# Kernel tuning notes

Measured on AMD Instinct MI355X. Metric: run time of the kernel, lower is better.

Reference implementation:

```python
import jax, jax.numpy as jnp
import numpy as np
import math

INF = 10000000000.0
D_KEY = 64


def setup_inputs() -> dict:
    key = jax.random.key(0)
    kq, kk, kv = jax.random.split(key, 3)
    B, S, D = 4, 4096, D_KEY
    return {
        "query": jax.random.normal(kq, (B, S, D), dtype=jnp.float32),
        "key": jax.random.normal(kk, (B, S, D), dtype=jnp.float32),
        "value": jax.random.normal(kv, (B, S, D), dtype=jnp.float32),
    }


def reference(query, key, value):
    # dot_products: [B, Sq, Sk]
    scale = math.sqrt(D_KEY)
    scores = jnp.einsum("bqd,bkd->bqk", query, key)
    S = key.shape[1]
    # causal: subtract INF on strict upper triangle (triu(1)), before scaling
    tri = jnp.triu(jnp.full((S, S), INF, dtype=scores.dtype), k=1)
    scores = scores - tri[None, :, :]
    logits = scores / scale
    probs = jax.nn.softmax(logits, axis=-1)  # softmax over key dim
    # dropout p=0.0 -> identity
    return jnp.einsum("bqk,bkd->bqd", probs, value)
```

## Files before the change

### kernel.cpp

```cpp
#include <hip/hip_runtime.h>
#include <hip/hip_bf16.h>
#include <math.h>

#define B_  4
#define S_  4096
#define D_  64
#define NQT 64
#define NST 32
#define QSC 0.18033688f
#define M0  20.0f

typedef __attribute__((ext_vector_type(8))) short bf16x8;
typedef __attribute__((ext_vector_type(4))) float f32x4;
typedef __attribute__((ext_vector_type(4))) short short4v;

static __device__ inline short f2bf(float f) {
    union { float f; unsigned u; } v; v.f = f;
    unsigned u = v.u;
    unsigned r = u + 0x7fff + ((u >> 16) & 1);
    return (short)(r >> 16);
}
static __device__ inline float bf2f(short s) {
    union { unsigned u; float f; } v; v.u = ((unsigned)(unsigned short)s) << 16;
    return v.f;
}
static __device__ inline unsigned cvt_pk_bf16(float lo, float hi) {
    unsigned r;
    asm("v_cvt_pk_bf16_f32 %0, %1, %2" : "=v"(r) : "v"(lo), "v"(hi));
    return r;
}
static __device__ inline void gload_lds16(const void* g, void* l) {
    __builtin_amdgcn_global_load_lds(
        (const __attribute__((address_space(1))) unsigned int*)g,
        (__attribute__((address_space(3))) unsigned int*)l,
        16, 0, 0);
}

__global__ __launch_bounds__(256) void fa_prep(const float* __restrict__ K,
                                               const float* __restrict__ V,
                                               short* __restrict__ Kbf,
                                               short* __restrict__ Vtbf)
{
    const int b   = blockIdx.x >> 6;
    const int st  = blockIdx.x & 63;
    const int tid = threadIdx.x;
    __shared__ short Vs[64 * 72];

    const size_t tbase = ((size_t)b * S_ + (size_t)st * 64) * D_;
    #pragma unroll
    for (int rr = 0; rr < 4; ++rr) {
        int i = tid + rr * 256;
        size_t e = tbase + (size_t)i * 4;
        f32x4 k = *(const f32x4*)(K + e);
        union { short4v s; unsigned u[2]; } ks;
        ks.u[0] = cvt_pk_bf16(k[0], k[1]);
        ks.u[1] = cvt_pk_bf16(k[2], k[3]);
        int key = i >> 4, d4 = (i & 15) * 4;
        int d4s = (((d4 >> 3) ^ (key & 7)) << 3) + (d4 & 7);
        *(short4v*)(Kbf + tbase + (size_t)key * 64 + d4s) = ks.s;
        f32x4 v = *(const f32x4*)(V + e);
        int slot = (key & 32) + (((key & 15) >> 2) << 3) + (((key >> 4) & 1) << 2) + (key & 3);
        Vs[(d4 + 0) * 72 + slot] = f2bf(v[0]);
        Vs[(d4 + 1) * 72 + slot] = f2bf(v[1]);
        Vs[(d4 + 2) * 72 + slot] = f2bf(v[2]);
        Vs[(d4 + 3) * 72 + slot] = f2bf(v[3]);
    }
    __syncthreads();
    #pragma unroll
    for (int cc = 0; cc < 2; ++cc) {
        int c = tid + cc * 256;
        int d = c >> 3, sg = c & 7;
        bf16x8 row = *(const bf16x8*)&Vs[d * 72 + sg * 8];
        *(bf16x8*)(Vtbf + ((size_t)(b * D_ + d)) * S_ + (size_t)st * 64 + (sg ^ (d & 7)) * 8) = row;
    }
}

__global__ __launch_bounds__(512, 6) void fa_part(const float* __restrict__ Qf,
                                               const short* __restrict__ Kbf,
                                               const short* __restrict__ Vtbf,
                                               short* __restrict__ Opart,
                                               float* __restrict__ Lpart,
                                               int CH, int T)
{
    const int bid = blockIdx.x;
    const int b   = bid / T;
    int r = bid - b * T;
    int qt2 = NST - 1;
    while (true) {
        int n = (2 * qt2 + 2 + CH - 1) / CH;
        if (r < n) break;
        r -= n; --qt2;
    }
    const int kt0 = r * CH;
    const int nkt = 2 * qt2 + 2;
    const int kt1 = (kt0 + CH < nkt) ? kt0 + CH : nkt;

    const int tid  = threadIdx.x;
    const int wave = tid >> 6;
    const int lane = tid & 63;
    const int lm   = lane & 15;
    const int lk   = lane >> 4;

    __shared__ __align__(16) short Ks[2][64 * 64];
    __shared__ __align__(16) short Vt[2][64 * 64];

    bf16x8 qA[2];
    {
        const float* qp = Qf + ((size_t)(b * S_ + qt2 * 128 + wave * 16 + lm)) * D_;
        #pragma unroll
        for (int h = 0; h < 2; ++h) {
            f32x4 a0 = *(const f32x4*)(qp + h * 32 + lk * 8);
            f32x4 a1 = *(const f32x4*)(qp + h * 32 + lk * 8 + 4);
            union { bf16x8 v; unsigned u[4]; } qa;
            qa.u[0] = cvt_pk_bf16(a0[0] * QSC, a0[1] * QSC);
            qa.u[1] = cvt_pk_bf16(a0[2] * QSC, a0[3] * QSC);
            qa.u[2] = cvt_pk_bf16(a1[0] * QSC, a1[1] * QSC);
            qa.u[3] = cvt_pk_bf16(a1[2] * QSC, a1[3] * QSC);
            qA[h] = qa.v;
        }
    }

    bf16x8 onesF;
    #pragma unroll
    for (int j = 0; j < 8; ++j) onesF[j] = (short)0x3F80;

    const char* kgp = (const char*)(Kbf + (size_t)b * S_ * D_)
                    + (size_t)kt0 * 8192 + tid * 16;
    const char* vgp = (const char*)(Vtbf + ((size_t)(b * D_ + (tid >> 3))) * S_)
                    + (size_t)kt0 * 128 + (tid & 7) * 16;

    gload_lds16(kgp, &Ks[0][wave * 512]);
    gload_lds16(vgp, &Vt[0][wave * 512]);
    kgp += 8192; vgp += 128;
    __syncthreads();

    f32x4 l4 = (f32x4){0.f, 0.f, 0.f, 0.f};
    f32x4 o_acc[4];
    #pragma unroll
    for (int dt = 0; dt < 4; ++dt) o_acc[dt] = (f32x4){0.f, 0.f, 0.f, 0.f};

    const int wrow = wave * 16 + lk * 4;
    const int qrow = wave * 16 + lm;
    int cur = 0;

    for (int kt = kt0; kt < kt1; ++kt) {
        if (kt + 1 < kt1) {
            gload_lds16(kgp, &Ks[cur ^ 1][wave * 512]);
            gload_lds16(vgp, &Vt[cur ^ 1][wave * 512]);
            kgp += 8192; vgp += 128;
        }

        f32x4 s4[4];
        __builtin_amdgcn_s_setprio(1);
        #pragma unroll
        for (int ct = 0; ct < 4; ++ct) {
            f32x4 acc = (f32x4){-M0, -M0, -M0, -M0};
            #pragma unroll
            for (int h = 0; h < 2; ++h) {
                int seg = (h * 4 + lk) ^ (lm & 7);
                bf16x8 kF = *(const bf16x8*)&Ks[cur][(ct * 16 + lm) * 64 + seg * 8];
                acc = __builtin_amdgcn_mfma_f32_16x16x32_bf16(kF, qA[h], acc, 0, 0, 0);
            }
            s4[ct] = acc;
        }
        __builtin_amdgcn_s_setprio(0);

        if (kt >= 2 * qt2) {
            const int koff = kt * 64 - qt2 * 128 + lk * 4;
            #pragma unroll
            for (int ct = 0; ct < 4; ++ct) {
                #pragma unroll
                for (int rr = 0; rr < 4; ++rr) {
                    if (koff + ct * 16 + rr > qrow) s4[ct][rr] = -INFINITY;
                }
            }
        }

        #pragma unroll
        for (int ct = 0; ct < 4; ++ct) {
            #pragma unroll
            for (int rr = 0; rr < 4; ++rr) s4[ct][rr] = exp2f(s4[ct][rr]);
        }
        bf16x8 aF[2];
        #pragma unroll
        for (int kh = 0; kh < 2; ++kh) {
            union { bf16x8 v; unsigned u[4]; } pa;
            pa.u[0] = cvt_pk_bf16(s4[2 * kh][0],     s4[2 * kh][1]);
            pa.u[1] = cvt_pk_bf16(s4[2 * kh][2],     s4[2 * kh][3]);
            pa.u[2] = cvt_pk_bf16(s4[2 * kh + 1][0], s4[2 * kh + 1][1]);
            pa.u[3] = cvt_pk_bf16(s4[2 * kh + 1][2], s4[2 * kh + 1][3]);
            aF[kh] = pa.v;
        }
        __builtin_amdgcn_s_setprio(1);
        #pragma unroll
        for (int kh = 0; kh < 2; ++kh)
            l4 = __builtin_amdgcn_mfma_f32_16x16x32_bf16(aF[kh], onesF, l4, 0, 0, 0);
        #pragma unroll
        for (int dt = 0; dt < 4; ++dt) {
            #pragma unroll
            for (int kh = 0; kh < 2; ++kh) {
                int seg = (kh * 4 + lk) ^ (lm & 7);
                bf16x8 bF = *(const bf16x8*)&Vt[cur][(dt * 16 + lm) * 64 + seg * 8];
                o_acc[dt] = __builtin_amdgcn_mfma_f32_16x16x32_bf16(aF[kh], bF, o_acc[dt], 0, 0, 0);
            }
        }
        __builtin_amdgcn_s_setprio(0);

        if (kt + 1 < kt1) {
            __syncthreads();
            cur ^= 1;
        }
    }

    short* Op = Opart + (size_t)bid * (128 * D_);
    if (lm == 0) {
        #pragma unroll
        for (int rr = 0; rr < 4; ++rr)
            Lpart[(size_t)bid * 128 + wrow + rr] = l4[rr];
    }
    #pragma unroll
    for (int dt = 0; dt < 4; ++dt) {
        unsigned o01 = cvt_pk_bf16(o_acc[dt][0], o_acc[dt][1]);
        unsigned o23 = cvt_pk_bf16(o_acc[dt][2], o_acc[dt][3]);
        Op[(wrow + 0) * D_ + dt * 16 + lm] = (short)(o01 & 0xffff);
        Op[(wrow + 1) * D_ + dt * 16 + lm] = (short)(o01 >> 16);
        Op[(wrow + 2) * D_ + dt * 16 + lm] = (short)(o23 & 0xffff);
        Op[(wrow + 3) * D_ + dt * 16 + lm] = (short)(o23 >> 16);
    }
}

__global__ __launch_bounds__(256) void fa_combine(const short* __restrict__ Opart,
                                                  const float* __restrict__ Lpart,
                                                  float* __restrict__ O,
                                                  int CH, int T)
{
    const int idx = blockIdx.x * 256 + threadIdx.x;
    const int b   = idx / (S_ * 16);
    const int rem = idx - b * (S_ * 16);
    const int q   = rem >> 4;
    const int d4  = (rem & 15) << 2;
    const int qt2 = q >> 7;
    const int rit = q & 127;

    int F = 0;
    for (int y = qt2 + 1; y < NST; ++y) F += (2 * y + 2 + CH - 1) / CH;
    const int base = b * T + F;
    const int nch  = (2 * qt2 + 2 + CH - 1) / CH;

    float L = 0.f;
    f32x4 acc = (f32x4){0.f, 0.f, 0.f, 0.f};
    for (int c = 0; c < nch; ++c) {
        L += Lpart[(size_t)(base + c) * 128 + rit];
        short4v o = *(const short4v*)(Opart + (size_t)(base + c) * (128 * D_) + rit * D_ + d4);
        acc[0] += bf2f(o[0]); acc[1] += bf2f(o[1]);
        acc[2] += bf2f(o[2]); acc[3] += bf2f(o[3]);
    }
    float inv = 1.f / L;
    f32x4 outv;
    outv[0] = acc[0] * inv; outv[1] = acc[1] * inv;
    outv[2] = acc[2] * inv; outv[3] = acc[3] * inv;
    *(f32x4*)(O + (size_t)idx * 4) = outv;
}

__global__ __launch_bounds__(256) void fa_fwd(const float* __restrict__ Q,
                                              const float* __restrict__ K,
                                              const float* __restrict__ V,
                                              float* __restrict__ O)
{
    const int qt   = (gridDim.x - 1) - blockIdx.x;
    const int b    = blockIdx.y;
    const int tid  = threadIdx.x;
    const int wave = tid >> 6;
    const int lane = tid & 63;
    const int lm   = lane & 15;
    const int lk   = lane >> 4;

    __shared__ short Ks[64 * 72];
    __shared__ short Vt[64 * 72];
    __shared__ short Ps[64 * 72];

    const float* Qb = Q + ((size_t)b * S_ + (size_t)qt * 64) * D_;
    const float* Kb = K + (size_t)b * S_ * D_;
    const float* Vb = V + (size_t)b * S_ * D_;

    bf16x8 qA[2];
    {
        const float* qp = Qb + (wave * 16 + lm) * D_;
        #pragma unroll
        for (int h = 0; h < 2; ++h) {
            const float* p = qp + h * 32 + lk * 8;
            #pragma unroll
            for (int j = 0; j < 8; ++j) qA[h][j] = f2bf(p[j] * 0.125f);
        }
    }
    float m_i[4], l_i[4];
    f32x4 o_acc[4];
    #pragma unroll
    for (int rr = 0; rr < 4; ++rr) { m_i[rr] = -INFINITY; l_i[rr] = 0.f; }
    #pragma unroll
    for (int dt = 0; dt < 4; ++dt) o_acc[dt] = (f32x4){0.f, 0.f, 0.f, 0.f};

    const int n_kt = qt + 1;
    for (int kt = 0; kt < n_kt; ++kt) {
        __syncthreads();
        #pragma unroll
        for (int rr = 0; rr < 4; ++rr) {
            int i   = tid + rr * 256;
            int row = i >> 4;
            int c4  = (i & 15) * 4;
            const size_t gbase = ((size_t)(kt * 64 + row)) * D_ + c4;
            f32x4 kv = *(const f32x4*)(Kb + gbase);
            short4v ks;
            ks[0] = f2bf(kv[0]); ks[1] = f2bf(kv[1]);
            ks[2] = f2bf(kv[2]); ks[3] = f2bf(kv[3]);
            *(short4v*)&Ks[row * 72 + c4] = ks;
            f32x4 vv = *(const f32x4*)(Vb + gbase);
            Vt[(c4 + 0) * 72 + row] = f2bf(vv[0]);
            Vt[(c4 + 1) * 72 + row] = f2bf(vv[1]);
            Vt[(c4 + 2) * 72 + row] = f2bf(vv[2]);
            Vt[(c4 + 3) * 72 + row] = f2bf(vv[3]);
        }
        __syncthreads();
        f32x4 s4[4];
        #pragma unroll
        for (int ct = 0; ct < 4; ++ct) {
            f32x4 acc = (f32x4){0.f, 0.f, 0.f, 0.f};
            #pragma unroll
            for (int h = 0; h < 2; ++h) {
                bf16x8 bF = *(const bf16x8*)&Ks[(ct * 16 + lm) * 72 + h * 32 + lk * 8];
                acc = __builtin_amdgcn_mfma_f32_16x16x32_bf16(qA[h], bF, acc, 0, 0, 0);
            }
            s4[ct] = acc;
        }
        if (kt == qt) {
            #pragma unroll
            for (int ct = 0; ct < 4; ++ct) {
                #pragma unroll
                for (int rr = 0; rr < 4; ++rr) {
                    int qrow = wave * 16 + lk * 4 + rr;
                    int kcol = ct * 16 + lm;
                    if (kcol > qrow) s4[ct][rr] = -INFINITY;
                }
            }
        }
        float alpha[4];
        #pragma unroll
        for (int rr = 0; rr < 4; ++rr) {
            float mx = fmaxf(fmaxf(s4[0][rr], s4[1][rr]), fmaxf(s4[2][rr], s4[3][rr]));
            mx = fmaxf(mx, __shfl_xor(mx, 1));
            mx = fmaxf(mx, __shfl_xor(mx, 2));
            mx = fmaxf(mx, __shfl_xor(mx, 4));
            mx = fmaxf(mx, __shfl_xor(mx, 8));
            float mn = fmaxf(m_i[rr], mx);
            alpha[rr] = __expf(m_i[rr] - mn);
            m_i[rr] = mn;
        }
        float rsum[4] = {0.f, 0.f, 0.f, 0.f};
        #pragma unroll
        for (int ct = 0; ct < 4; ++ct) {
            #pragma unroll
            for (int rr = 0; rr < 4; ++rr) {
                float p = __expf(s4[ct][rr] - m_i[rr]);
                s4[ct][rr] = p;
                rsum[rr] += p;
            }
        }
        #pragma unroll
        for (int rr = 0; rr < 4; ++rr) {
            float rs = rsum[rr];
            rs += __shfl_xor(rs, 1);
            rs += __shfl_xor(rs, 2);
            rs += __shfl_xor(rs, 4);
            rs += __shfl_xor(rs, 8);
            l_i[rr] = l_i[rr] * alpha[rr] + rs;
        }
        #pragma unroll
        for (int ct = 0; ct < 4; ++ct) {
            #pragma unroll
            for (int rr = 0; rr < 4; ++rr) {
                Ps[(wave * 16 + lk * 4 + rr) * 72 + ct * 16 + lm] = f2bf(s4[ct][rr]);
            }
        }
        #pragma unroll
        for (int dt = 0; dt < 4; ++dt) {
            #pragma unroll
            for (int rr = 0; rr < 4; ++rr) o_acc[dt][rr] *= alpha[rr];
        }
        #pragma unroll
        for (int dt = 0; dt < 4; ++dt) {
            #pragma unroll
            for (int kh = 0; kh < 2; ++kh) {
                bf16x8 aF = *(const bf16x8*)&Ps[(wave * 16 + lm) * 72 + kh * 32 + lk * 8];
                bf16x8 bF = *(const bf16x8*)&Vt[(dt * 16 + lm) * 72 + kh * 32 + lk * 8];
                o_acc[dt] = __builtin_amdgcn_mfma_f32_16x16x32_bf16(aF, bF, o_acc[dt], 0, 0, 0);
            }
        }
    }
    float* Ob = O + ((size_t)b * S_ + (size_t)qt * 64) * D_;
    #pragma unroll
    for (int rr = 0; rr < 4; ++rr) {
        float inv = 1.f / l_i[rr];
        int row = wave * 16 + lk * 4 + rr;
        #pragma unroll
        for (int dt = 0; dt < 4; ++dt) {
            Ob[row * D_ + dt * 16 + lm] = o_acc[dt][rr] * inv;
        }
    }
}

extern "C" void kernel_launch(void* const* d_in, const int* in_sizes, int n_in,
                              void* d_out, int out_size, void* d_ws, size_t ws_size,
                              hipStream_t stream) {
    const float* Q = (const float*)d_in[0];
    const float* K = (const float*)d_in[1];
    const float* V = (const float*)d_in[2];
    float* O = (float*)d_out;

    const size_t convShorts = (size_t)B_ * S_ * D_;
    int CH = 0, T = 0;
    const int chs[5] = {6, 8, 16, 32, 64};
    for (int k = 0; k < 5; ++k) {
        int c = chs[k];
        int t = 0;
        for (int q2 = 0; q2 < NST; ++q2) t += (2 * q2 + 2 + c - 1) / c;
        size_t need = 2 * convShorts * 2
                    + (size_t)B_ * t * (128 * D_) * 2
                    + (size_t)B_ * t * 128 * 4;
        if (need <= ws_size) { CH = c; T = t; break; }
    }
    if (CH == 0) {
        dim3 grid(NQT, B_);
        fa_fwd<<<grid, 256, 0, stream>>>(Q, K, V, O);
        return;
    }
    short* Kbf   = (short*)d_ws;
    short* Vtbf  = Kbf + convShorts;
    short* Opart = Vtbf + convShorts;
    float* Lpart = (float*)(Opart + (size_t)B_ * T * (128 * D_));

    fa_prep<<<dim3(B_ * NQT), 256, 0, stream>>>(K, V, Kbf, Vtbf);
    fa_part<<<dim3(B_ * T), 512, 0, stream>>>(Q, Kbf, Vtbf, Opart, Lpart, CH, T);
    fa_combine<<<dim3((B_ * S_ * 16) / 256), 256, 0, stream>>>(Opart, Lpart, O, CH, T);
}
```

Baseline: 94.69 us.

## Process two query row groups per wave and stage K/V through registers

The partial-attention kernel now runs 4 waves of 256 threads, each handling 32 query rows (two 16-row groups), so every K and V fragment read from LDS feeds two MFMAs. This is meant to halve LDS read traffic per MFMA and to raise instruction-level parallelism. The asynchronous global-to-LDS loads are replaced by register prefetch of the next tile, which is written to LDS after compute. The trade-off is more accumulator registers per wave, fewer waves per block, and the LDS writes now sitting on the critical path before the barrier.

```diff
diff --git a/kernel.cpp b/kernel.cpp
--- a/kernel.cpp
+++ b/kernel.cpp
@@ -28,12 +28,6 @@
     unsigned r;
     asm("v_cvt_pk_bf16_f32 %0, %1, %2" : "=v"(r) : "v"(lo), "v"(hi));
     return r;
-}
-static __device__ inline void gload_lds16(const void* g, void* l) {
-    __builtin_amdgcn_global_load_lds(
-        (const __attribute__((address_space(1))) unsigned int*)g,
-        (__attribute__((address_space(3))) unsigned int*)l,
-        16, 0, 0);
 }
 
 __global__ __launch_bounds__(256) void fa_prep(const float* __restrict__ K,
@@ -75,7 +69,7 @@
     }
 }
 
-__global__ __launch_bounds__(512, 6) void fa_part(const float* __restrict__ Qf,
+__global__ __launch_bounds__(256, 3) void fa_part(const float* __restrict__ Qf,
                                                const short* __restrict__ Kbf,
                                                const short* __restrict__ Vtbf,
                                                short* __restrict__ Opart,
@@ -104,9 +98,10 @@
     __shared__ __align__(16) short Ks[2][64 * 64];
     __shared__ __align__(16) short Vt[2][64 * 64];
 
-    bf16x8 qA[2];
-    {
-        const float* qp = Qf + ((size_t)(b * S_ + qt2 * 128 + wave * 16 + lm)) * D_;
+    bf16x8 qA[2][2];
+    #pragma unroll
+    for (int g = 0; g < 2; ++g) {
+        const float* qp = Qf + ((size_t)(b * S_ + qt2 * 128 + wave * 32 + g * 16 + lm)) * D_;
         #pragma unroll
         for (int h = 0; h < 2; ++h) {
             f32x4 a0 = *(const f32x4*)(qp + h * 32 + lk * 8);
@@ -116,7 +111,7 @@
             qa.u[1] = cvt_pk_bf16(a0[2] * QSC, a0[3] * QSC);
             qa.u[2] = cvt_pk_bf16(a1[0] * QSC, a1[1] * QSC);
             qa.u[3] = cvt_pk_bf16(a1[2] * QSC, a1[3] * QSC);
-            qA[h] = qa.v;
+            qA[g][h] = qa.v;
         }
     }
 
@@ -124,108 +119,141 @@
     #pragma unroll
     for (int j = 0; j < 8; ++j) onesF[j] = (short)0x3F80;
 
-    const char* kgp = (const char*)(Kbf + (size_t)b * S_ * D_)
-                    + (size_t)kt0 * 8192 + tid * 16;
-    const char* vgp = (const char*)(Vtbf + ((size_t)(b * D_ + (tid >> 3))) * S_)
-                    + (size_t)kt0 * 128 + (tid & 7) * 16;
-
-    gload_lds16(kgp, &Ks[0][wave * 512]);
-    gload_lds16(vgp, &Vt[0][wave * 512]);
-    kgp += 8192; vgp += 128;
+    const short* Kb = Kbf + (size_t)b * S_ * D_;
+    const short* Vb = Vtbf + (size_t)b * D_ * S_;
+    const short* kS0 = Kb + (size_t)kt0 * 4096 + tid * 8;
+    const short* kS1 = kS0 + 2048;
+    const short* vS0 = Vb + (size_t)(tid >> 3) * S_ + kt0 * 64 + (tid & 7) * 8;
+    const short* vS1 = vS0 + (size_t)32 * S_;
+
+    bf16x8 kr0 = *(const bf16x8*)kS0, kr1 = *(const bf16x8*)kS1;
+    bf16x8 vr0 = *(const bf16x8*)vS0, vr1 = *(const bf16x8*)vS1;
+    kS0 += 4096; kS1 += 4096; vS0 += 64; vS1 += 64;
+    *(bf16x8*)&Ks[0][tid * 8]        = kr0;
+    *(bf16x8*)&Ks[0][2048 + tid * 8] = kr1;
+    *(bf16x8*)&Vt[0][tid * 8]        = vr0;
+    *(bf16x8*)&Vt[0][2048 + tid * 8] = vr1;
     __syncthreads();
-
-    f32x4 l4 = (f32x4){0.f, 0.f, 0.f, 0.f};
-    f32x4 o_acc[4];
-    #pragma unroll
-    for (int dt = 0; dt < 4; ++dt) o_acc[dt] = (f32x4){0.f, 0.f, 0.f, 0.f};
-
-    const int wrow = wave * 16 + lk * 4;
-    const int qrow = wave * 16 + lm;
+    if (kt0 + 1 < kt1) {
+        kr0 = *(const bf16x8*)kS0; kr1 = *(const bf16x8*)kS1;
+        vr0 = *(const bf16x8*)vS0; vr1 = *(const bf16x8*)vS1;
+        kS0 += 4096; kS1 += 4096; vS0 += 64; vS1 += 64;
+    }
+
+    f32x4 l4[2];
+    l4[0] = (f32x4){0.f, 0.f, 0.f, 0.f};
+    l4[1] = (f32x4){0.f, 0.f, 0.f, 0.f};
+    f32x4 o_acc[2][4];
+    #pragma unroll
+    for (int g = 0; g < 2; ++g)
+        #pragma unroll
+        for (int dt = 0; dt < 4; ++dt) o_acc[g][dt] = (f32x4){0.f, 0.f, 0.f, 0.f};
+
+    const int qrow0 = wave * 32 + lm;
     int cur = 0;
 
     for (int kt = kt0; kt < kt1; ++kt) {
-        if (kt + 1 < kt1) {
-            gload_lds16(kgp, &Ks[cur ^ 1][wave * 512]);
-            gload_lds16(vgp, &Vt[cur ^ 1][wave * 512]);
-            kgp += 8192; vgp += 128;
-        }
-
-        f32x4 s4[4];
+        f32x4 s4[2][4];
         __builtin_amdgcn_s_setprio(1);
         #pragma unroll
         for (int ct = 0; ct < 4; ++ct) {
-            f32x4 acc = (f32x4){-M0, -M0, -M0, -M0};
+            s4[0][ct] = (f32x4){-M0, -M0, -M0, -M0};
+            s4[1][ct] = (f32x4){-M0, -M0, -M0, -M0};
             #pragma unroll
             for (int h = 0; h < 2; ++h) {
                 int seg = (h * 4 + lk) ^ (lm & 7);
                 bf16x8 kF = *(const bf16x8*)&Ks[cur][(ct * 16 + lm) * 64 + seg * 8];
-                acc = __builtin_amdgcn_mfma_f32_16x16x32_bf16(kF, qA[h], acc, 0, 0, 0);
-            }
-            s4[ct] = acc;
+                s4[0][ct] = __builtin_amdgcn_mfma_f32_16x16x32_bf16(kF, qA[0][h], s4[0][ct], 0, 0, 0);
+                s4[1][ct] = __builtin_amdgcn_mfma_f32_16x16x32_bf16(kF, qA[1][h], s4[1][ct], 0, 0, 0);
+            }
         }
         __builtin_amdgcn_s_setprio(0);
 
         if (kt >= 2 * qt2) {
             const int koff = kt * 64 - qt2 * 128 + lk * 4;
             #pragma unroll
-            for (int ct = 0; ct < 4; ++ct) {
+            for (int g = 0; g < 2; ++g) {
                 #pragma unroll
-                for (int rr = 0; rr < 4; ++rr) {
-                    if (koff + ct * 16 + rr > qrow) s4[ct][rr] = -INFINITY;
+                for (int ct = 0; ct < 4; ++ct) {
+                    #pragma unroll
+                    for (int rr = 0; rr < 4; ++rr) {
+                        if (koff + ct * 16 + rr > qrow0 + g * 16) s4[g][ct][rr] = -INFINITY;
+                    }
                 }
             }
         }
 
         #pragma unroll
-        for (int ct = 0; ct < 4; ++ct) {
-            #pragma unroll
-            for (int rr = 0; rr < 4; ++rr) s4[ct][rr] = exp2f(s4[ct][rr]);
-        }
-        bf16x8 aF[2];
-        #pragma unroll
-        for (int kh = 0; kh < 2; ++kh) {
-            union { bf16x8 v; unsigned u[4]; } pa;
-            pa.u[0] = cvt_pk_bf16(s4[2 * kh][0],     s4[2 * kh][1]);
-            pa.u[1] = cvt_pk_bf16(s4[2 * kh][2],     s4[2 * kh][3]);
-            pa.u[2] = cvt_pk_bf16(s4[2 * kh + 1][0], s4[2 * kh + 1][1]);
-            pa.u[3] = cvt_pk_bf16(s4[2 * kh + 1][2], s4[2 * kh + 1][3]);
-            aF[kh] = pa.v;
+        for (int g = 0; g < 2; ++g)
+            #pragma unroll
+            for (int ct = 0; ct < 4; ++ct)
+                #pragma unroll
+                for (int rr = 0; rr < 4; ++rr) s4[g][ct][rr] = exp2f(s4[g][ct][rr]);
+
+        bf16x8 aF[2][2];
+        #pragma unroll
+        for (int g = 0; g < 2; ++g) {
+            #pragma unroll
+            for (int kh = 0; kh < 2; ++kh) {
+                union { bf16x8 v; unsigned u[4]; } pa;
+                pa.u[0] = cvt_pk_bf16(s4[g][2 * kh][0],     s4[g][2 * kh][1]);
+                pa.u[1] = cvt_pk_bf16(s4[g][2 * kh][2],     s4[g][2 * kh][3]);
+                pa.u[2] = cvt_pk_bf16(s4[g][2 * kh + 1][0], s4[g][2 * kh + 1][1]);
+                pa.u[3] = cvt_pk_bf16(s4[g][2 * kh + 1][2], s4[g][2 * kh + 1][3]);
+                aF[g][kh] = pa.v;
+            }
         }
         __builtin_amdgcn_s_setprio(1);
         #pragma unroll
-        for (int kh = 0; kh < 2; ++kh)
-            l4 = __builtin_amdgcn_mfma_f32_16x16x32_bf16(aF[kh], onesF, l4, 0, 0, 0);
+        for (int g = 0; g < 2; ++g)
+            #pragma unroll
+            for (int kh = 0; kh < 2; ++kh)
+                l4[g] = __builtin_amdgcn_mfma_f32_16x16x32_bf16(aF[g][kh], onesF, l4[g], 0, 0, 0);
         #pragma unroll
         for (int dt = 0; dt < 4; ++dt) {
             #pragma unroll
             for (int kh = 0; kh < 2; ++kh) {
                 int seg = (kh * 4 + lk) ^ (lm & 7);
                 bf16x8 bF = *(const bf16x8*)&Vt[cur][(dt * 16 + lm) * 64 + seg * 8];
-                o_acc[dt] = __builtin_amdgcn_mfma_f32_16x16x32_bf16(aF[kh], bF, o_acc[dt], 0, 0, 0);
+                o_acc[0][dt] = __builtin_amdgcn_mfma_f32_16x16x32_bf16(aF[0][kh], bF, o_acc[0][dt], 0, 0, 0);
+                o_acc[1][dt] = __builtin_amdgcn_mfma_f32_16x16x32_bf16(aF[1][kh], bF, o_acc[1][dt], 0, 0, 0);
             }
         }
         __builtin_amdgcn_s_setprio(0);
 
         if (kt + 1 < kt1) {
+            *(bf16x8*)&Ks[cur ^ 1][tid * 8]        = kr0;
+            *(bf16x8*)&Ks[cur ^ 1][2048 + tid * 8] = kr1;
+            *(bf16x8*)&Vt[cur ^ 1][tid * 8]        = vr0;
+            *(bf16x8*)&Vt[cur ^ 1][2048 + tid * 8] = vr1;
             __syncthreads();
+            if (kt + 2 < kt1) {
+                kr0 = *(const bf16x8*)kS0; kr1 = *(const bf16x8*)kS1;
+                vr0 = *(const bf16x8*)vS0; vr1 = *(const bf16x8*)vS1;
+                kS0 += 4096; kS1 += 4096; vS0 += 64; vS1 += 64;
+            }
             cur ^= 1;
         }
     }
 
     short* Op = Opart + (size_t)bid * (128 * D_);
-    if (lm == 0) {
-        #pragma unroll
-        for (int rr = 0; rr < 4; ++rr)
-            Lpart[(size_t)bid * 128 + wrow + rr] = l4[rr];
-    }
-    #pragma unroll
-    for (int dt = 0; dt < 4; ++dt) {
-        unsigned o01 = cvt_pk_bf16(o_acc[dt][0], o_acc[dt][1]);
-        unsigned o23 = cvt_pk_bf16(o_acc[dt][2], o_acc[dt][3]);
-        Op[(wrow + 0) * D_ + dt * 16 + lm] = (short)(o01 & 0xffff);
-        Op[(wrow + 1) * D_ + dt * 16 + lm] = (short)(o01 >> 16);
-        Op[(wrow + 2) * D_ + dt * 16 + lm] = (short)(o23 & 0xffff);
-        Op[(wrow + 3) * D_ + dt * 16 + lm] = (short)(o23 >> 16);
+    #pragma unroll
+    for (int g = 0; g < 2; ++g) {
+        const int wrow = wave * 32 + g * 16 + lk * 4;
+        if (lm == 0) {
+            #pragma unroll
+            for (int rr = 0; rr < 4; ++rr)
+                Lpart[(size_t)bid * 128 + wrow + rr] = l4[g][rr];
+        }
+        #pragma unroll
+        for (int dt = 0; dt < 4; ++dt) {
+            unsigned o01 = cvt_pk_bf16(o_acc[g][dt][0], o_acc[g][dt][1]);
+            unsigned o23 = cvt_pk_bf16(o_acc[g][dt][2], o_acc[g][dt][3]);
+            Op[(wrow + 0) * D_ + dt * 16 + lm] = (short)(o01 & 0xffff);
+            Op[(wrow + 1) * D_ + dt * 16 + lm] = (short)(o01 >> 16);
+            Op[(wrow + 2) * D_ + dt * 16 + lm] = (short)(o23 & 0xffff);
+            Op[(wrow + 3) * D_ + dt * 16 + lm] = (short)(o23 >> 16);
+        }
     }
 }
 
@@ -439,6 +467,6 @@
     float* Lpart = (float*)(Opart + (size_t)B_ * T * (128 * D_));
 
     fa_prep<<<dim3(B_ * NQT), 256, 0, stream>>>(K, V, Kbf, Vtbf);
-    fa_part<<<dim3(B_ * T), 512, 0, stream>>>(Q, Kbf, Vtbf, Opart, Lpart, CH, T);
+    fa_part<<<dim3(B_ * T), 256, 0, stream>>>(Q, Kbf, Vtbf, Opart, Lpart, CH, T);
     fa_combine<<<dim3((B_ * S_ * 16) / 256), 256, 0, stream>>>(Opart, Lpart, O, CH, T);
 }
```

After: 93.47 us. Within noise of the previous version (-1.3%).
